# Optimization experiments

Measured on AMD Instinct MI355X. Metric: run time of the kernel, lower is better.

The kernel has to match this reference:

```python
import jax, jax.numpy as jnp
import numpy as np

EPS = 1e-06
K = 4          # hc_mult
D = 2048       # hidden_size
SINKHORN_ITERS = 20


def setup_inputs() -> dict:
    key = jax.random.key(0)
    k1, k2, k3 = jax.random.split(key, 3)
    B, S = 2, 4096
    x = jax.random.normal(k1, (B, S, K, D), dtype=jnp.float32)
    out = jax.random.normal(k2, (B, S, D), dtype=jnp.float32)
    out_dim = (2 + K) * K  # 24
    # matches nn.init.normal_(std=1/sqrt(K*D))
    W = jax.random.normal(k3, (out_dim, K * D), dtype=jnp.float32) / np.sqrt(K * D)
    scale = jnp.ones((3,), dtype=jnp.float32)
    base = jnp.zeros((out_dim,), dtype=jnp.float32)
    return {"x": x, "out": out, "W": W, "scale": scale, "base": base}


def _sinkhorn(m, n_iters=SINKHORN_ITERS, eps=EPS):
    # one priming column normalization, then (n_iters-1) row/col cycles
    m = m / (jnp.sum(m, axis=-2, keepdims=True) + eps)
    for _ in range(max(n_iters - 1, 0)):
        m = m / (jnp.sum(m, axis=-1, keepdims=True) + eps)
        m = m / (jnp.sum(m, axis=-2, keepdims=True) + eps)
    return m


def reference(x, out, W, scale, base):
    out_dtype = x.dtype
    # --- _packed_logits: flatten K streams, RMS-normalize, project (fp32) ---
    flat = x.reshape(*x.shape[:-2], K * D).astype(jnp.float32)      # [B,S,K*D]
    rsqrt = jax.lax.rsqrt(jnp.mean(flat * flat, axis=-1, keepdims=True) + EPS)
    logits = jnp.einsum('bsf,of->bso', flat * rsqrt, W)             # [B,S,24]
    # --- compute_weights: split into pre/post/comb ---
    pre_logit = logits[..., :K] * scale[0] + base[:K]
    post_logit = logits[..., K:2 * K] * scale[1] + base[K:2 * K]
    comb_logit = (logits[..., 2 * K:].reshape(*logits.shape[:-1], K, K) * scale[2]
                  + base[2 * K:].reshape(K, K))
    pre = jax.nn.sigmoid(pre_logit) + EPS                           # [B,S,K]
    post = 2.0 * jax.nn.sigmoid(post_logit)                         # [B,S,K]
    comb = jax.nn.softmax(comb_logit, axis=-1) + EPS                # [B,S,K,K]
    comb = _sinkhorn(comb)                                          # doubly-stochastic
    pre = pre.astype(out_dtype)
    post = post.astype(out_dtype)
    comb = comb.astype(out_dtype)
    # --- collapse: K streams -> 1 via pre weights ---
    collapsed = jnp.sum(pre[..., None] * x, axis=-2)                # [B,S,D]
    # --- expand: write sub-block output back to K streams ---
    write = post[..., None] * out[..., None, :]                     # [B,S,K,D]
    mix = jnp.einsum('bshk,bskd->bshd', comb, x)                    # [B,S,K,D]
    y = write + mix
    return (y, collapsed)
```

## Files before the change

kernel.cpp:

```cpp
#include <hip/hip_runtime.h>


#define EPS 1e-6f
constexpr int K_ = 4, D_ = 2048, KD = 8192, NOUT = 24;
constexpr int NTOK = 2 * 4096;
constexpr int TPB = 512;
constexpr int TOKS = 4;
constexpr int NBLK = NTOK / TOKS;

typedef _Float16 h2 __attribute__((ext_vector_type(2)));

static __device__ __forceinline__ unsigned int pk2(float a, float b) {
    h2 h; h.x = (_Float16)a; h.y = (_Float16)b;
    return __builtin_bit_cast(unsigned int, h);
}

static __device__ __forceinline__ float dot2(unsigned int w, unsigned int x, float c) {
#if __has_builtin(__builtin_amdgcn_fdot2)
    return __builtin_amdgcn_fdot2(__builtin_bit_cast(h2, w),
                                  __builtin_bit_cast(h2, x), c, false);
#else
    h2 hw = __builtin_bit_cast(h2, w), hx = __builtin_bit_cast(h2, x);
    return c + (float)hw.x * (float)hx.x + (float)hw.y * (float)hx.y;
#endif
}

static __device__ __forceinline__ float frcp(float v) {
#if __has_builtin(__builtin_amdgcn_rcpf)
    return __builtin_amdgcn_rcpf(v);
#else
    return 1.f / v;
#endif
}

__global__ void conv_w_kernel(const float* __restrict__ W, unsigned int* __restrict__ Wh) {
    int g = blockIdx.x * blockDim.x + threadIdx.x;
    const float* src = W + (size_t)g * 8;
    float4 a = *reinterpret_cast<const float4*>(src);
    float4 b = *reinterpret_cast<const float4*>(src + 4);
    uint4 u;
    u.x = pk2(a.x, a.y); u.y = pk2(a.z, a.w);
    u.z = pk2(b.x, b.y); u.w = pk2(b.z, b.w);
    *reinterpret_cast<uint4*>(Wh + (size_t)g * 4) = u;
}

__global__ __launch_bounds__(TPB, 2) void hypermix_kernel(
    const float* __restrict__ x, const float* __restrict__ outp,
    const unsigned int* __restrict__ Wh,
    const float* __restrict__ scale, const float* __restrict__ base,
    float* __restrict__ y, float* __restrict__ coll)
{
    const int t = threadIdx.x;
    const int w = t >> 6, lane = t & 63;
    const size_t gt0 = (size_t)blockIdx.x * TOKS;

    __shared__ unsigned int xh[TOKS][KD / 2];
    __shared__ float ssred[TOKS][8];
    __shared__ float lg[TOKS][24];
    __shared__ float wts[TOKS][24];

    float4 ovr[4];
#pragma unroll 2
    for (int tt = 0; tt < TOKS; ++tt) {
        const float* xb = x + (gt0 + tt) * KD + t * 4;
        float4 v[4];
#pragma unroll
        for (int i = 0; i < 4; ++i)
            v[i] = *reinterpret_cast<const float4*>(xb + i * 2048);
        ovr[tt] = *reinterpret_cast<const float4*>(outp + (gt0 + tt) * D_ + t * 4);
        float ss = 0.f;
#pragma unroll
        for (int i = 0; i < 4; ++i) {
            ss += v[i].x * v[i].x + v[i].y * v[i].y + v[i].z * v[i].z + v[i].w * v[i].w;
            uint2 p; p.x = pk2(v[i].x, v[i].y); p.y = pk2(v[i].z, v[i].w);
            *reinterpret_cast<uint2*>(&xh[tt][i * 1024 + t * 2]) = p;
        }
#pragma unroll
        for (int m = 1; m < 64; m <<= 1) ss += __shfl_xor(ss, m, 64);
        if (lane == 0) ssred[tt][w] = ss;
    }
    __syncthreads();

    {
        const int r0 = w * 3;
        const unsigned int* Wp0 = Wh + (size_t)(r0 + 0) * 4096;
        const unsigned int* Wp1 = Wh + (size_t)(r0 + 1) * 4096;
        const unsigned int* Wp2 = Wh + (size_t)(r0 + 2) * 4096;
        float acc[3][4];
#pragma unroll
        for (int j = 0; j < 3; ++j)
#pragma unroll
            for (int tt = 0; tt < 4; ++tt) acc[j][tt] = 0.f;

        uint4 xa0, xa1, xa2, xa3, wa0, wa1, wa2;
        uint4 xb0, xb1, xb2, xb3, wb0, wb1, wb2;

#define LOADIT(X0, X1, X2, X3, W0, W1, W2, IT) do {                          \
        const int gi4 = ((IT) * 64 + lane) * 4;                              \
        X0 = *reinterpret_cast<const uint4*>(&xh[0][gi4]);                   \
        X1 = *reinterpret_cast<const uint4*>(&xh[1][gi4]);                   \
        X2 = *reinterpret_cast<const uint4*>(&xh[2][gi4]);                   \
        X3 = *reinterpret_cast<const uint4*>(&xh[3][gi4]);                   \
        W0 = *reinterpret_cast<const uint4*>(Wp0 + gi4);                     \
        W1 = *reinterpret_cast<const uint4*>(Wp1 + gi4);                     \
        W2 = *reinterpret_cast<const uint4*>(Wp2 + gi4);                     \
    } while (0)
#define DOT4(A, WV, XV) do {                                                 \
        A = dot2(WV.x, XV.x, A); A = dot2(WV.y, XV.y, A);                    \
        A = dot2(WV.z, XV.z, A); A = dot2(WV.w, XV.w, A);                    \
    } while (0)
#define CONSUME(X0, X1, X2, X3, W0, W1, W2) do {                             \
        DOT4(acc[0][0], W0, X0); DOT4(acc[0][1], W0, X1);                    \
        DOT4(acc[0][2], W0, X2); DOT4(acc[0][3], W0, X3);                    \
        DOT4(acc[1][0], W1, X0); DOT4(acc[1][1], W1, X1);                    \
        DOT4(acc[1][2], W1, X2); DOT4(acc[1][3], W1, X3);                    \
        DOT4(acc[2][0], W2, X0); DOT4(acc[2][1], W2, X1);                    \
        DOT4(acc[2][2], W2, X2); DOT4(acc[2][3], W2, X3);                    \
    } while (0)

        LOADIT(xa0, xa1, xa2, xa3, wa0, wa1, wa2, 0);
#pragma unroll 1
        for (int it2 = 0; it2 < 7; ++it2) {
            LOADIT(xb0, xb1, xb2, xb3, wb0, wb1, wb2, 2 * it2 + 1);
            CONSUME(xa0, xa1, xa2, xa3, wa0, wa1, wa2);
            LOADIT(xa0, xa1, xa2, xa3, wa0, wa1, wa2, 2 * it2 + 2);
            CONSUME(xb0, xb1, xb2, xb3, wb0, wb1, wb2);
        }
        LOADIT(xb0, xb1, xb2, xb3, wb0, wb1, wb2, 15);
        CONSUME(xa0, xa1, xa2, xa3, wa0, wa1, wa2);
        CONSUME(xb0, xb1, xb2, xb3, wb0, wb1, wb2);
#undef LOADIT
#undef DOT4
#undef CONSUME

#pragma unroll
        for (int j = 0; j < 3; ++j)
#pragma unroll
            for (int tt = 0; tt < 4; ++tt) {
                float v = acc[j][tt];
#pragma unroll
                for (int m = 1; m < 64; m <<= 1) v += __shfl_xor(v, m, 64);
                if (lane == 0) lg[tt][r0 + j] = v;
            }
    }
    __syncthreads();

    if (t < TOKS) {
        float ss = ssred[t][0] + ssred[t][1] + ssred[t][2] + ssred[t][3]
                 + ssred[t][4] + ssred[t][5] + ssred[t][6] + ssred[t][7];
        float rms = rsqrtf(ss * (1.f / 8192.f) + EPS);
        float s0 = scale[0], s1 = scale[1], s2 = scale[2];
        float l[24];
#pragma unroll
        for (int i = 0; i < 24; ++i) l[i] = lg[t][i];
#pragma unroll
        for (int k = 0; k < 4; ++k) {
            float z0 = l[k] * rms * s0 + base[k];
            wts[t][k] = frcp(1.f + __expf(-z0)) + EPS;
            float z1 = l[4 + k] * rms * s1 + base[4 + k];
            wts[t][4 + k] = 2.f * frcp(1.f + __expf(-z1));
        }
        float p[16];
#pragma unroll
        for (int h = 0; h < 4; ++h) {
            float c0 = l[8 + h * 4 + 0] * rms * s2 + base[8 + h * 4 + 0];
            float c1 = l[8 + h * 4 + 1] * rms * s2 + base[8 + h * 4 + 1];
            float c2 = l[8 + h * 4 + 2] * rms * s2 + base[8 + h * 4 + 2];
            float c3 = l[8 + h * 4 + 3] * rms * s2 + base[8 + h * 4 + 3];
            float mx = fmaxf(fmaxf(c0, c1), fmaxf(c2, c3));
            float e0 = __expf(c0 - mx), e1 = __expf(c1 - mx);
            float e2 = __expf(c2 - mx), e3 = __expf(c3 - mx);
            float inv = frcp(e0 + e1 + e2 + e3);
            p[h * 4 + 0] = e0 * inv + EPS; p[h * 4 + 1] = e1 * inv + EPS;
            p[h * 4 + 2] = e2 * inv + EPS; p[h * 4 + 3] = e3 * inv + EPS;
        }
#pragma unroll
        for (int k = 0; k < 4; ++k) {
            float inv = frcp(p[k] + p[4 + k] + p[8 + k] + p[12 + k] + EPS);
            p[k] *= inv; p[4 + k] *= inv; p[8 + k] *= inv; p[12 + k] *= inv;
        }
#pragma unroll 1
        for (int itn = 0; itn < 19; ++itn) {
#pragma unroll
            for (int h = 0; h < 4; ++h) {
                float inv = frcp(p[h * 4] + p[h * 4 + 1] + p[h * 4 + 2] + p[h * 4 + 3] + EPS);
                p[h * 4] *= inv; p[h * 4 + 1] *= inv; p[h * 4 + 2] *= inv; p[h * 4 + 3] *= inv;
            }
#pragma unroll
            for (int k = 0; k < 4; ++k) {
                float inv = frcp(p[k] + p[4 + k] + p[8 + k] + p[12 + k] + EPS);
                p[k] *= inv; p[4 + k] *= inv; p[8 + k] *= inv; p[12 + k] *= inv;
            }
        }
#pragma unroll
        for (int i = 0; i < 16; ++i) wts[t][8 + i] = p[i];
    }
    __syncthreads();

#pragma unroll 1
    for (int tt = 0; tt < TOKS; ++tt) {
        float pre[4], post[4], cmb[4][4];
#pragma unroll
        for (int k = 0; k < 4; ++k) { pre[k] = wts[tt][k]; post[k] = wts[tt][4 + k]; }
#pragma unroll
        for (int h = 0; h < 4; ++h)
#pragma unroll
            for (int k = 0; k < 4; ++k) cmb[h][k] = wts[tt][8 + h * 4 + k];

        const int d = t * 4;
        float xk[4][4];
#pragma unroll
        for (int k = 0; k < 4; ++k) {
            uint2 pq = *reinterpret_cast<const uint2*>(&xh[tt][k * 1024 + t * 2]);
            h2 h0 = __builtin_bit_cast(h2, pq.x), h1 = __builtin_bit_cast(h2, pq.y);
            xk[k][0] = (float)h0.x; xk[k][1] = (float)h0.y;
            xk[k][2] = (float)h1.x; xk[k][3] = (float)h1.y;
        }
        float* yb = y + (gt0 + tt) * KD;
        float* cb = coll + (gt0 + tt) * D_;
        float cv[4], yv[4];
#pragma unroll
        for (int e = 0; e < 4; ++e)
            cv[e] = pre[0] * xk[0][e] + pre[1] * xk[1][e]
                  + pre[2] * xk[2][e] + pre[3] * xk[3][e];
        *reinterpret_cast<float4*>(cb + d) = make_float4(cv[0], cv[1], cv[2], cv[3]);
        const float oe[4] = {ovr[tt].x, ovr[tt].y, ovr[tt].z, ovr[tt].w};
#pragma unroll
        for (int h = 0; h < 4; ++h) {
#pragma unroll
            for (int e = 0; e < 4; ++e)
                yv[e] = post[h] * oe[e] + cmb[h][0] * xk[0][e] + cmb[h][1] * xk[1][e]
                      + cmb[h][2] * xk[2][e] + cmb[h][3] * xk[3][e];
            *reinterpret_cast<float4*>(yb + h * D_ + d) =
                make_float4(yv[0], yv[1], yv[2], yv[3]);
        }
    }
}

extern "C" void kernel_launch(void* const* d_in, const int* in_sizes, int n_in,
                              void* d_out, int out_size, void* d_ws, size_t ws_size,
                              hipStream_t stream) {
    const float* x     = (const float*)d_in[0];
    const float* outp  = (const float*)d_in[1];
    const float* W     = (const float*)d_in[2];
    const float* scale = (const float*)d_in[3];
    const float* base  = (const float*)d_in[4];
    float* y    = (float*)d_out;
    float* coll = y + (size_t)NTOK * KD;

    unsigned int* Wh = (unsigned int*)d_ws;
    conv_w_kernel<<<NOUT * KD / 8 / 256, 256, 0, stream>>>(W, Wh);
    hypermix_kernel<<<NBLK, TPB, 0, stream>>>(x, outp, Wh, scale, base, y, coll);
}
```

Before: 195.6 us.

## Make hypermix kernel persistent with async LDS prefetch and double-buffered conversion

Launches a fixed grid of 256 blocks, each looping over 16 groups of two tokens instead of one block per four tokens. Uses global_load_lds to stream the next token pair's x into an LDS staging buffer while the current pair's projection and output run. Conversion to fp16 and the sum of squares for the following group are done into a second buffer, overlapped with the weight computation. The aim is to hide global load latency and amortise launch and setup work. The cost is much larger LDS use (about 128 KB), one block per CU with fewer waves to hide memory latency, and extra barriers per group.

```diff
diff --git a/kernel.cpp b/kernel.cpp
--- a/kernel.cpp
+++ b/kernel.cpp
@@ -2,11 +2,12 @@
 
 
 #define EPS 1e-6f
-constexpr int K_ = 4, D_ = 2048, KD = 8192, NOUT = 24;
-constexpr int NTOK = 2 * 4096;
+constexpr int D_ = 2048, KD = 8192, NOUT = 24;
+constexpr int NTOK = 8192;
 constexpr int TPB = 512;
-constexpr int TOKS = 4;
-constexpr int NBLK = NTOK / TOKS;
+constexpr int TPG = 2;
+constexpr int NBLK = 256;
+constexpr int NG = NTOK / (NBLK * TPG);
 
 typedef _Float16 h2 __attribute__((ext_vector_type(2)));
 
@@ -44,7 +45,7 @@
     *reinterpret_cast<uint4*>(Wh + (size_t)g * 4) = u;
 }
 
-__global__ __launch_bounds__(TPB, 2) void hypermix_kernel(
+__global__ __launch_bounds__(TPB) void hypermix_kernel(
     const float* __restrict__ x, const float* __restrict__ outp,
     const unsigned int* __restrict__ Wh,
     const float* __restrict__ scale, const float* __restrict__ base,
@@ -52,153 +53,95 @@
 {
     const int t = threadIdx.x;
     const int w = t >> 6, lane = t & 63;
-    const size_t gt0 = (size_t)blockIdx.x * TOKS;
-
-    __shared__ unsigned int xh[TOKS][KD / 2];
-    __shared__ float ssred[TOKS][8];
-    __shared__ float lg[TOKS][24];
-    __shared__ float wts[TOKS][24];
-
-    float4 ovr[4];
-#pragma unroll 2
-    for (int tt = 0; tt < TOKS; ++tt) {
-        const float* xb = x + (gt0 + tt) * KD + t * 4;
-        float4 v[4];
-#pragma unroll
-        for (int i = 0; i < 4; ++i)
-            v[i] = *reinterpret_cast<const float4*>(xb + i * 2048);
-        ovr[tt] = *reinterpret_cast<const float4*>(outp + (gt0 + tt) * D_ + t * 4);
-        float ss = 0.f;
-#pragma unroll
-        for (int i = 0; i < 4; ++i) {
-            ss += v[i].x * v[i].x + v[i].y * v[i].y + v[i].z * v[i].z + v[i].w * v[i].w;
-            uint2 p; p.x = pk2(v[i].x, v[i].y); p.y = pk2(v[i].z, v[i].w);
-            *reinterpret_cast<uint2*>(&xh[tt][i * 1024 + t * 2]) = p;
-        }
-#pragma unroll
-        for (int m = 1; m < 64; m <<= 1) ss += __shfl_xor(ss, m, 64);
-        if (lane == 0) ssred[tt][w] = ss;
-    }
-    __syncthreads();
-
-    {
-        const int r0 = w * 3;
-        const unsigned int* Wp0 = Wh + (size_t)(r0 + 0) * 4096;
-        const unsigned int* Wp1 = Wh + (size_t)(r0 + 1) * 4096;
-        const unsigned int* Wp2 = Wh + (size_t)(r0 + 2) * 4096;
-        float acc[3][4];
-#pragma unroll
-        for (int j = 0; j < 3; ++j)
-#pragma unroll
-            for (int tt = 0; tt < 4; ++tt) acc[j][tt] = 0.f;
-
-        uint4 xa0, xa1, xa2, xa3, wa0, wa1, wa2;
-        uint4 xb0, xb1, xb2, xb3, wb0, wb1, wb2;
-
-#define LOADIT(X0, X1, X2, X3, W0, W1, W2, IT) do {                          \
-        const int gi4 = ((IT) * 64 + lane) * 4;                              \
-        X0 = *reinterpret_cast<const uint4*>(&xh[0][gi4]);                   \
-        X1 = *reinterpret_cast<const uint4*>(&xh[1][gi4]);                   \
-        X2 = *reinterpret_cast<const uint4*>(&xh[2][gi4]);                   \
-        X3 = *reinterpret_cast<const uint4*>(&xh[3][gi4]);                   \
-        W0 = *reinterpret_cast<const uint4*>(Wp0 + gi4);                     \
-        W1 = *reinterpret_cast<const uint4*>(Wp1 + gi4);                     \
-        W2 = *reinterpret_cast<const uint4*>(Wp2 + gi4);                     \
-    } while (0)
-#define DOT4(A, WV, XV) do {                                                 \
-        A = dot2(WV.x, XV.x, A); A = dot2(WV.y, XV.y, A);                    \
-        A = dot2(WV.z, XV.z, A); A = dot2(WV.w, XV.w, A);                    \
-    } while (0)
-#define CONSUME(X0, X1, X2, X3, W0, W1, W2) do {                             \
-        DOT4(acc[0][0], W0, X0); DOT4(acc[0][1], W0, X1);                    \
-        DOT4(acc[0][2], W0, X2); DOT4(acc[0][3], W0, X3);                    \
-        DOT4(acc[1][0], W1, X0); DOT4(acc[1][1], W1, X1);                    \
-        DOT4(acc[1][2], W1, X2); DOT4(acc[1][3], W1, X3);                    \
-        DOT4(acc[2][0], W2, X0); DOT4(acc[2][1], W2, X1);                    \
-        DOT4(acc[2][2], W2, X2); DOT4(acc[2][3], W2, X3);                    \
-    } while (0)
-
-        LOADIT(xa0, xa1, xa2, xa3, wa0, wa1, wa2, 0);
-#pragma unroll 1
-        for (int it2 = 0; it2 < 7; ++it2) {
-            LOADIT(xb0, xb1, xb2, xb3, wb0, wb1, wb2, 2 * it2 + 1);
-            CONSUME(xa0, xa1, xa2, xa3, wa0, wa1, wa2);
-            LOADIT(xa0, xa1, xa2, xa3, wa0, wa1, wa2, 2 * it2 + 2);
-            CONSUME(xb0, xb1, xb2, xb3, wb0, wb1, wb2);
-        }
-        LOADIT(xb0, xb1, xb2, xb3, wb0, wb1, wb2, 15);
-        CONSUME(xa0, xa1, xa2, xa3, wa0, wa1, wa2);
-        CONSUME(xb0, xb1, xb2, xb3, wb0, wb1, wb2);
-#undef LOADIT
-#undef DOT4
-#undef CONSUME
-
-#pragma unroll
-        for (int j = 0; j < 3; ++j)
-#pragma unroll
-            for (int tt = 0; tt < 4; ++tt) {
-                float v = acc[j][tt];
-#pragma unroll
-                for (int m = 1; m < 64; m <<= 1) v += __shfl_xor(v, m, 64);
-                if (lane == 0) lg[tt][r0 + j] = v;
-            }
-    }
-    __syncthreads();
-
-    if (t < TOKS) {
-        float ss = ssred[t][0] + ssred[t][1] + ssred[t][2] + ssred[t][3]
-                 + ssred[t][4] + ssred[t][5] + ssred[t][6] + ssred[t][7];
-        float rms = rsqrtf(ss * (1.f / 8192.f) + EPS);
-        float s0 = scale[0], s1 = scale[1], s2 = scale[2];
-        float l[24];
-#pragma unroll
-        for (int i = 0; i < 24; ++i) l[i] = lg[t][i];
-#pragma unroll
-        for (int k = 0; k < 4; ++k) {
-            float z0 = l[k] * rms * s0 + base[k];
-            wts[t][k] = frcp(1.f + __expf(-z0)) + EPS;
-            float z1 = l[4 + k] * rms * s1 + base[4 + k];
-            wts[t][4 + k] = 2.f * frcp(1.f + __expf(-z1));
-        }
-        float p[16];
-#pragma unroll
-        for (int h = 0; h < 4; ++h) {
-            float c0 = l[8 + h * 4 + 0] * rms * s2 + base[8 + h * 4 + 0];
-            float c1 = l[8 + h * 4 + 1] * rms * s2 + base[8 + h * 4 + 1];
-            float c2 = l[8 + h * 4 + 2] * rms * s2 + base[8 + h * 4 + 2];
-            float c3 = l[8 + h * 4 + 3] * rms * s2 + base[8 + h * 4 + 3];
-            float mx = fmaxf(fmaxf(c0, c1), fmaxf(c2, c3));
-            float e0 = __expf(c0 - mx), e1 = __expf(c1 - mx);
-            float e2 = __expf(c2 - mx), e3 = __expf(c3 - mx);
-            float inv = frcp(e0 + e1 + e2 + e3);
-            p[h * 4 + 0] = e0 * inv + EPS; p[h * 4 + 1] = e1 * inv + EPS;
-            p[h * 4 + 2] = e2 * inv + EPS; p[h * 4 + 3] = e3 * inv + EPS;
-        }
-#pragma unroll
-        for (int k = 0; k < 4; ++k) {
-            float inv = frcp(p[k] + p[4 + k] + p[8 + k] + p[12 + k] + EPS);
-            p[k] *= inv; p[4 + k] *= inv; p[8 + k] *= inv; p[12 + k] *= inv;
-        }
-#pragma unroll 1
-        for (int itn = 0; itn < 19; ++itn) {
+    const size_t tok0 = (size_t)blockIdx.x * (NG * TPG);
+
+    __shared__ float stage[TPG * KD];
+    __shared__ unsigned int xh[2][TPG][KD / 2];
+    __shared__ float ssred[2][4];
+    __shared__ float lg[TPG][NOUT];
+    __shared__ float wts[TPG][NOUT];
+
+    auto PREF = [&](int gr) {
+        const float* gsrc = x + (tok0 + (size_t)gr * TPG) * KD;
+#pragma unroll
+        for (int i = 0; i < 8; ++i)
+            __builtin_amdgcn_global_load_lds(
+                (const __attribute__((address_space(1))) unsigned int*)(gsrc + (i * 512 + t) * 4),
+                (__attribute__((address_space(3))) unsigned int*)(&stage[(i * 512 + t) * 4]),
+                16, 0, 0);
+    };
+
+    auto CONVERT = [&](int buf) {
+        if (w < 4) {
+            const int tk = t >> 7, cl = t & 127;
+            float ss = 0.f;
+#pragma unroll 4
+            for (int i = 0; i < 16; ++i) {
+                float4 a = *reinterpret_cast<const float4*>(&stage[tk * KD + cl * 4 + i * 512]);
+                ss += a.x * a.x + a.y * a.y + a.z * a.z + a.w * a.w;
+                uint2 p; p.x = pk2(a.x, a.y); p.y = pk2(a.z, a.w);
+                *reinterpret_cast<uint2*>(&xh[buf][tk][cl * 2 + i * 256]) = p;
+            }
+#pragma unroll
+            for (int m = 1; m < 64; m <<= 1) ss += __shfl_xor(ss, m, 64);
+            if (lane == 0) ssred[buf][w] = ss;
+        }
+    };
+
+    auto WEIGHTS = [&](int cur) {
+        if (w == 7 && lane < TPG) {
+            const int tk = lane;
+            float ss = ssred[cur][2 * tk] + ssred[cur][2 * tk + 1];
+            float rms = rsqrtf(ss * (1.f / 8192.f) + EPS);
+            float s0 = scale[0], s1 = scale[1], s2 = scale[2];
+            float l[24];
+#pragma unroll
+            for (int i = 0; i < 24; ++i) l[i] = lg[tk][i];
+#pragma unroll
+            for (int k = 0; k < 4; ++k) {
+                float z0 = l[k] * rms * s0 + base[k];
+                wts[tk][k] = frcp(1.f + __expf(-z0)) + EPS;
+                float z1 = l[4 + k] * rms * s1 + base[4 + k];
+                wts[tk][4 + k] = 2.f * frcp(1.f + __expf(-z1));
+            }
+            float p[16];
 #pragma unroll
             for (int h = 0; h < 4; ++h) {
-                float inv = frcp(p[h * 4] + p[h * 4 + 1] + p[h * 4 + 2] + p[h * 4 + 3] + EPS);
-                p[h * 4] *= inv; p[h * 4 + 1] *= inv; p[h * 4 + 2] *= inv; p[h * 4 + 3] *= inv;
+                float c0 = l[8 + h * 4 + 0] * rms * s2 + base[8 + h * 4 + 0];
+                float c1 = l[8 + h * 4 + 1] * rms * s2 + base[8 + h * 4 + 1];
+                float c2 = l[8 + h * 4 + 2] * rms * s2 + base[8 + h * 4 + 2];
+                float c3 = l[8 + h * 4 + 3] * rms * s2 + base[8 + h * 4 + 3];
+                float mx = fmaxf(fmaxf(c0, c1), fmaxf(c2, c3));
+                float e0 = __expf(c0 - mx), e1 = __expf(c1 - mx);
+                float e2 = __expf(c2 - mx), e3 = __expf(c3 - mx);
+                float inv = frcp(e0 + e1 + e2 + e3);
+                p[h * 4 + 0] = e0 * inv + EPS; p[h * 4 + 1] = e1 * inv + EPS;
+                p[h * 4 + 2] = e2 * inv + EPS; p[h * 4 + 3] = e3 * inv + EPS;
             }
 #pragma unroll
             for (int k = 0; k < 4; ++k) {
                 float inv = frcp(p[k] + p[4 + k] + p[8 + k] + p[12 + k] + EPS);
                 p[k] *= inv; p[4 + k] *= inv; p[8 + k] *= inv; p[12 + k] *= inv;
             }
-        }
-#pragma unroll
-        for (int i = 0; i < 16; ++i) wts[t][8 + i] = p[i];
-    }
-    __syncthreads();
-
 #pragma unroll 1
-    for (int tt = 0; tt < TOKS; ++tt) {
+            for (int itn = 0; itn < 19; ++itn) {
+#pragma unroll
+                for (int h = 0; h < 4; ++h) {
+                    float inv = frcp(p[h * 4] + p[h * 4 + 1] + p[h * 4 + 2] + p[h * 4 + 3] + EPS);
+                    p[h * 4] *= inv; p[h * 4 + 1] *= inv; p[h * 4 + 2] *= inv; p[h * 4 + 3] *= inv;
+                }
+#pragma unroll
+                for (int k = 0; k < 4; ++k) {
+                    float inv = frcp(p[k] + p[4 + k] + p[8 + k] + p[12 + k] + EPS);
+                    p[k] *= inv; p[4 + k] *= inv; p[8 + k] *= inv; p[12 + k] *= inv;
+                }
+            }
+#pragma unroll
+            for (int i = 0; i < 16; ++i) wts[tk][8 + i] = p[i];
+        }
+    };
+
+    auto PHB = [&](int tt, int cur, const float4& ov, size_t gtok) {
         float pre[4], post[4], cmb[4][4];
 #pragma unroll
         for (int k = 0; k < 4; ++k) { pre[k] = wts[tt][k]; post[k] = wts[tt][4 + k]; }
@@ -206,25 +149,24 @@
         for (int h = 0; h < 4; ++h)
 #pragma unroll
             for (int k = 0; k < 4; ++k) cmb[h][k] = wts[tt][8 + h * 4 + k];
-
         const int d = t * 4;
         float xk[4][4];
 #pragma unroll
         for (int k = 0; k < 4; ++k) {
-            uint2 pq = *reinterpret_cast<const uint2*>(&xh[tt][k * 1024 + t * 2]);
+            uint2 pq = *reinterpret_cast<const uint2*>(&xh[cur][tt][k * 1024 + t * 2]);
             h2 h0 = __builtin_bit_cast(h2, pq.x), h1 = __builtin_bit_cast(h2, pq.y);
             xk[k][0] = (float)h0.x; xk[k][1] = (float)h0.y;
             xk[k][2] = (float)h1.x; xk[k][3] = (float)h1.y;
         }
-        float* yb = y + (gt0 + tt) * KD;
-        float* cb = coll + (gt0 + tt) * D_;
+        float* yb = y + gtok * KD;
+        float* cb = coll + gtok * D_;
         float cv[4], yv[4];
 #pragma unroll
         for (int e = 0; e < 4; ++e)
             cv[e] = pre[0] * xk[0][e] + pre[1] * xk[1][e]
                   + pre[2] * xk[2][e] + pre[3] * xk[3][e];
         *reinterpret_cast<float4*>(cb + d) = make_float4(cv[0], cv[1], cv[2], cv[3]);
-        const float oe[4] = {ovr[tt].x, ovr[tt].y, ovr[tt].z, ovr[tt].w};
+        const float oe[4] = {ov.x, ov.y, ov.z, ov.w};
 #pragma unroll
         for (int h = 0; h < 4; ++h) {
 #pragma unroll
@@ -234,6 +176,64 @@
             *reinterpret_cast<float4*>(yb + h * D_ + d) =
                 make_float4(yv[0], yv[1], yv[2], yv[3]);
         }
+    };
+
+    PREF(0);
+    __syncthreads();
+    CONVERT(0);
+    __syncthreads();
+    PREF(1);
+
+#pragma unroll 1
+    for (int g = 0; g < NG; ++g) {
+        const int cur = g & 1;
+        const size_t gt = tok0 + (size_t)g * TPG;
+        float4 ovr0 = *reinterpret_cast<const float4*>(outp + gt * D_ + t * 4);
+        float4 ovr1 = *reinterpret_cast<const float4*>(outp + (gt + 1) * D_ + t * 4);
+
+        {
+            const int r0 = w * 3;
+            float acc[3][2] = {};
+#pragma unroll 2
+            for (int it = 0; it < 16; ++it) {
+                const int gi4 = (it * 64 + lane) * 4;
+                uint4 xa = *reinterpret_cast<const uint4*>(&xh[cur][0][gi4]);
+                uint4 xb = *reinterpret_cast<const uint4*>(&xh[cur][1][gi4]);
+#pragma unroll
+                for (int j = 0; j < 3; ++j) {
+                    uint4 wv = *reinterpret_cast<const uint4*>(
+                        Wh + (size_t)(r0 + j) * 4096 + gi4);
+                    acc[j][0] = dot2(wv.x, xa.x, acc[j][0]);
+                    acc[j][0] = dot2(wv.y, xa.y, acc[j][0]);
+                    acc[j][0] = dot2(wv.z, xa.z, acc[j][0]);
+                    acc[j][0] = dot2(wv.w, xa.w, acc[j][0]);
+                    acc[j][1] = dot2(wv.x, xb.x, acc[j][1]);
+                    acc[j][1] = dot2(wv.y, xb.y, acc[j][1]);
+                    acc[j][1] = dot2(wv.z, xb.z, acc[j][1]);
+                    acc[j][1] = dot2(wv.w, xb.w, acc[j][1]);
+                }
+            }
+#pragma unroll
+            for (int j = 0; j < 3; ++j) {
+                float v0 = acc[j][0], v1 = acc[j][1];
+#pragma unroll
+                for (int m = 1; m < 64; m <<= 1) {
+                    v0 += __shfl_xor(v0, m, 64);
+                    v1 += __shfl_xor(v1, m, 64);
+                }
+                if (lane == 0) { lg[0][r0 + j] = v0; lg[1][r0 + j] = v1; }
+            }
+        }
+        __syncthreads();
+
+        if (g + 1 < NG) CONVERT(cur ^ 1);
+        WEIGHTS(cur);
+        __syncthreads();
+
+        if (g + 2 < NG) PREF(g + 2);
+
+        PHB(0, cur, ovr0, gt);
+        PHB(1, cur, ovr1, gt + 1);
     }
 }
 
```

New measurement: 240.9 us. 23.2% more time.

## Process three tokens per block with out staged in LDS and simpler GEMV loop

Applied to the files above, without the earlier changes.

Each block now handles three tokens instead of four, with bounds clamping for the ragged last block. All x and out loads for the block are issued together up front, and the out vector is staged in shared memory instead of registers. The explicit double-buffered projection loop is replaced by a plain unrolled loop, and the occupancy hint is dropped from launch bounds. The aim is more blocks in flight and less register pressure, in exchange for more blocks, extra LDS use and fewer tokens sharing each W load.

```diff
diff --git a/kernel.cpp b/kernel.cpp
--- a/kernel.cpp
+++ b/kernel.cpp
@@ -2,11 +2,11 @@
 
 
 #define EPS 1e-6f
-constexpr int K_ = 4, D_ = 2048, KD = 8192, NOUT = 24;
-constexpr int NTOK = 2 * 4096;
+constexpr int D_ = 2048, KD = 8192, NOUT = 24;
+constexpr int NTOK = 8192;
 constexpr int TPB = 512;
-constexpr int TOKS = 4;
-constexpr int NBLK = NTOK / TOKS;
+constexpr int TOKS = 3;
+constexpr int NBLK = (NTOK + TOKS - 1) / TOKS;
 
 typedef _Float16 h2 __attribute__((ext_vector_type(2)));
 
@@ -44,7 +44,7 @@
     *reinterpret_cast<uint4*>(Wh + (size_t)g * 4) = u;
 }
 
-__global__ __launch_bounds__(TPB, 2) void hypermix_kernel(
+__global__ __launch_bounds__(TPB) void hypermix_kernel(
     const float* __restrict__ x, const float* __restrict__ outp,
     const unsigned int* __restrict__ Wh,
     const float* __restrict__ scale, const float* __restrict__ base,
@@ -53,90 +53,100 @@
     const int t = threadIdx.x;
     const int w = t >> 6, lane = t & 63;
     const size_t gt0 = (size_t)blockIdx.x * TOKS;
+    const size_t tks0 = gt0;
+    const size_t tks1 = (gt0 + 1 < NTOK) ? gt0 + 1 : NTOK - 1;
+    const size_t tks2 = (gt0 + 2 < NTOK) ? gt0 + 2 : NTOK - 1;
 
     __shared__ unsigned int xh[TOKS][KD / 2];
+    __shared__ float os[TOKS][D_];
     __shared__ float ssred[TOKS][8];
     __shared__ float lg[TOKS][24];
     __shared__ float wts[TOKS][24];
 
-    float4 ovr[4];
-#pragma unroll 2
-    for (int tt = 0; tt < TOKS; ++tt) {
-        const float* xb = x + (gt0 + tt) * KD + t * 4;
-        float4 v[4];
-#pragma unroll
-        for (int i = 0; i < 4; ++i)
-            v[i] = *reinterpret_cast<const float4*>(xb + i * 2048);
-        ovr[tt] = *reinterpret_cast<const float4*>(outp + (gt0 + tt) * D_ + t * 4);
-        float ss = 0.f;
+    {
+        const float* xb0 = x + tks0 * KD + t * 4;
+        const float* xb1 = x + tks1 * KD + t * 4;
+        const float* xb2 = x + tks2 * KD + t * 4;
+        float4 a0[4], a1[4], a2[4];
+#pragma unroll
+        for (int i = 0; i < 4; ++i) a0[i] = *reinterpret_cast<const float4*>(xb0 + i * 2048);
+#pragma unroll
+        for (int i = 0; i < 4; ++i) a1[i] = *reinterpret_cast<const float4*>(xb1 + i * 2048);
+#pragma unroll
+        for (int i = 0; i < 4; ++i) a2[i] = *reinterpret_cast<const float4*>(xb2 + i * 2048);
+        float4 o0 = *reinterpret_cast<const float4*>(outp + tks0 * D_ + t * 4);
+        float4 o1 = *reinterpret_cast<const float4*>(outp + tks1 * D_ + t * 4);
+        float4 o2 = *reinterpret_cast<const float4*>(outp + tks2 * D_ + t * 4);
+
+        float ss0 = 0.f, ss1 = 0.f, ss2 = 0.f;
 #pragma unroll
         for (int i = 0; i < 4; ++i) {
-            ss += v[i].x * v[i].x + v[i].y * v[i].y + v[i].z * v[i].z + v[i].w * v[i].w;
-            uint2 p; p.x = pk2(v[i].x, v[i].y); p.y = pk2(v[i].z, v[i].w);
-            *reinterpret_cast<uint2*>(&xh[tt][i * 1024 + t * 2]) = p;
-        }
-#pragma unroll
-        for (int m = 1; m < 64; m <<= 1) ss += __shfl_xor(ss, m, 64);
-        if (lane == 0) ssred[tt][w] = ss;
+            ss0 += a0[i].x * a0[i].x + a0[i].y * a0[i].y + a0[i].z * a0[i].z + a0[i].w * a0[i].w;
+            uint2 p; p.x = pk2(a0[i].x, a0[i].y); p.y = pk2(a0[i].z, a0[i].w);
+            *reinterpret_cast<uint2*>(&xh[0][i * 1024 + t * 2]) = p;
+        }
+#pragma unroll
+        for (int i = 0; i < 4; ++i) {
+            ss1 += a1[i].x * a1[i].x + a1[i].y * a1[i].y + a1[i].z * a1[i].z + a1[i].w * a1[i].w;
+            uint2 p; p.x = pk2(a1[i].x, a1[i].y); p.y = pk2(a1[i].z, a1[i].w);
+            *reinterpret_cast<uint2*>(&xh[1][i * 1024 + t * 2]) = p;
+        }
+#pragma unroll
+        for (int i = 0; i < 4; ++i) {
+            ss2 += a2[i].x * a2[i].x + a2[i].y * a2[i].y + a2[i].z * a2[i].z + a2[i].w * a2[i].w;
+            uint2 p; p.x = pk2(a2[i].x, a2[i].y); p.y = pk2(a2[i].z, a2[i].w);
+            *reinterpret_cast<uint2*>(&xh[2][i * 1024 + t * 2]) = p;
+        }
+        *reinterpret_cast<float4*>(&os[0][t * 4]) = o0;
+        *reinterpret_cast<float4*>(&os[1][t * 4]) = o1;
+        *reinterpret_cast<float4*>(&os[2][t * 4]) = o2;
+
+#pragma unroll
+        for (int m = 1; m < 64; m <<= 1) {
+            ss0 += __shfl_xor(ss0, m, 64);
+            ss1 += __shfl_xor(ss1, m, 64);
+            ss2 += __shfl_xor(ss2, m, 64);
+        }
+        if (lane == 0) { ssred[0][w] = ss0; ssred[1][w] = ss1; ssred[2][w] = ss2; }
     }
     __syncthreads();
 
     {
         const int r0 = w * 3;
-        const unsigned int* Wp0 = Wh + (size_t)(r0 + 0) * 4096;
-        const unsigned int* Wp1 = Wh + (size_t)(r0 + 1) * 4096;
-        const unsigned int* Wp2 = Wh + (size_t)(r0 + 2) * 4096;
-        float acc[3][4];
+        float acc[3][TOKS];
 #pragma unroll
         for (int j = 0; j < 3; ++j)
 #pragma unroll
-            for (int tt = 0; tt < 4; ++tt) acc[j][tt] = 0.f;
-
-        uint4 xa0, xa1, xa2, xa3, wa0, wa1, wa2;
-        uint4 xb0, xb1, xb2, xb3, wb0, wb1, wb2;
-
-#define LOADIT(X0, X1, X2, X3, W0, W1, W2, IT) do {                          \
-        const int gi4 = ((IT) * 64 + lane) * 4;                              \
-        X0 = *reinterpret_cast<const uint4*>(&xh[0][gi4]);                   \
-        X1 = *reinterpret_cast<const uint4*>(&xh[1][gi4]);                   \
-        X2 = *reinterpret_cast<const uint4*>(&xh[2][gi4]);                   \
-        X3 = *reinterpret_cast<const uint4*>(&xh[3][gi4]);                   \
-        W0 = *reinterpret_cast<const uint4*>(Wp0 + gi4);                     \
-        W1 = *reinterpret_cast<const uint4*>(Wp1 + gi4);                     \
-        W2 = *reinterpret_cast<const uint4*>(Wp2 + gi4);                     \
-    } while (0)
-#define DOT4(A, WV, XV) do {                                                 \
-        A = dot2(WV.x, XV.x, A); A = dot2(WV.y, XV.y, A);                    \
-        A = dot2(WV.z, XV.z, A); A = dot2(WV.w, XV.w, A);                    \
-    } while (0)
-#define CONSUME(X0, X1, X2, X3, W0, W1, W2) do {                             \
-        DOT4(acc[0][0], W0, X0); DOT4(acc[0][1], W0, X1);                    \
-        DOT4(acc[0][2], W0, X2); DOT4(acc[0][3], W0, X3);                    \
-        DOT4(acc[1][0], W1, X0); DOT4(acc[1][1], W1, X1);                    \
-        DOT4(acc[1][2], W1, X2); DOT4(acc[1][3], W1, X3);                    \
-        DOT4(acc[2][0], W2, X0); DOT4(acc[2][1], W2, X1);                    \
-        DOT4(acc[2][2], W2, X2); DOT4(acc[2][3], W2, X3);                    \
-    } while (0)
-
-        LOADIT(xa0, xa1, xa2, xa3, wa0, wa1, wa2, 0);
-#pragma unroll 1
-        for (int it2 = 0; it2 < 7; ++it2) {
-            LOADIT(xb0, xb1, xb2, xb3, wb0, wb1, wb2, 2 * it2 + 1);
-            CONSUME(xa0, xa1, xa2, xa3, wa0, wa1, wa2);
-            LOADIT(xa0, xa1, xa2, xa3, wa0, wa1, wa2, 2 * it2 + 2);
-            CONSUME(xb0, xb1, xb2, xb3, wb0, wb1, wb2);
-        }
-        LOADIT(xb0, xb1, xb2, xb3, wb0, wb1, wb2, 15);
-        CONSUME(xa0, xa1, xa2, xa3, wa0, wa1, wa2);
-        CONSUME(xb0, xb1, xb2, xb3, wb0, wb1, wb2);
-#undef LOADIT
-#undef DOT4
-#undef CONSUME
-
+            for (int tt = 0; tt < TOKS; ++tt) acc[j][tt] = 0.f;
+
+#pragma unroll 2
+        for (int it = 0; it < 16; ++it) {
+            const int gi = it * 64 + lane;
+            uint4 xv0 = *reinterpret_cast<const uint4*>(&xh[0][gi * 4]);
+            uint4 xv1 = *reinterpret_cast<const uint4*>(&xh[1][gi * 4]);
+            uint4 xv2 = *reinterpret_cast<const uint4*>(&xh[2][gi * 4]);
+#pragma unroll
+            for (int j = 0; j < 3; ++j) {
+                uint4 wv = *reinterpret_cast<const uint4*>(
+                    Wh + ((size_t)(r0 + j) * 4096 + gi * 4));
+                acc[j][0] = dot2(wv.x, xv0.x, acc[j][0]);
+                acc[j][0] = dot2(wv.y, xv0.y, acc[j][0]);
+                acc[j][0] = dot2(wv.z, xv0.z, acc[j][0]);
+                acc[j][0] = dot2(wv.w, xv0.w, acc[j][0]);
+                acc[j][1] = dot2(wv.x, xv1.x, acc[j][1]);
+                acc[j][1] = dot2(wv.y, xv1.y, acc[j][1]);
+                acc[j][1] = dot2(wv.z, xv1.z, acc[j][1]);
+                acc[j][1] = dot2(wv.w, xv1.w, acc[j][1]);
+                acc[j][2] = dot2(wv.x, xv2.x, acc[j][2]);
+                acc[j][2] = dot2(wv.y, xv2.y, acc[j][2]);
+                acc[j][2] = dot2(wv.z, xv2.z, acc[j][2]);
+                acc[j][2] = dot2(wv.w, xv2.w, acc[j][2]);
+            }
+        }
 #pragma unroll
         for (int j = 0; j < 3; ++j)
 #pragma unroll
-            for (int tt = 0; tt < 4; ++tt) {
+            for (int tt = 0; tt < TOKS; ++tt) {
                 float v = acc[j][tt];
 #pragma unroll
                 for (int m = 1; m < 64; m <<= 1) v += __shfl_xor(v, m, 64);
@@ -145,7 +155,7 @@
     }
     __syncthreads();
 
-    if (t < TOKS) {
+    if (t < TOKS && gt0 + t < NTOK) {
         float ss = ssred[t][0] + ssred[t][1] + ssred[t][2] + ssred[t][3]
                  + ssred[t][4] + ssred[t][5] + ssred[t][6] + ssred[t][7];
         float rms = rsqrtf(ss * (1.f / 8192.f) + EPS);
@@ -199,6 +209,7 @@
 
 #pragma unroll 1
     for (int tt = 0; tt < TOKS; ++tt) {
+        if (gt0 + tt >= NTOK) continue;
         float pre[4], post[4], cmb[4][4];
 #pragma unroll
         for (int k = 0; k < 4; ++k) { pre[k] = wts[tt][k]; post[k] = wts[tt][4 + k]; }
@@ -216,6 +227,7 @@
             xk[k][0] = (float)h0.x; xk[k][1] = (float)h0.y;
             xk[k][2] = (float)h1.x; xk[k][3] = (float)h1.y;
         }
+        float4 ov = *reinterpret_cast<const float4*>(&os[tt][t * 4]);
         float* yb = y + (gt0 + tt) * KD;
         float* cb = coll + (gt0 + tt) * D_;
         float cv[4], yv[4];
@@ -224,7 +236,7 @@
             cv[e] = pre[0] * xk[0][e] + pre[1] * xk[1][e]
                   + pre[2] * xk[2][e] + pre[3] * xk[3][e];
         *reinterpret_cast<float4*>(cb + d) = make_float4(cv[0], cv[1], cv[2], cv[3]);
-        const float oe[4] = {ovr[tt].x, ovr[tt].y, ovr[tt].z, ovr[tt].w};
+        const float oe[4] = {ov.x, ov.y, ov.z, ov.w};
 #pragma unroll
         for (int h = 0; h < 4; ++h) {
 #pragma unroll
```

Measured after the change: 180.6 us. -7.7%, faster.
